# Kernel tuning notes

Hardware: AMD Instinct MI355X
Metric: run time of the kernel (lower is better)

Reference implementation:

```python
import jax, jax.numpy as jnp
import numpy as np

H, W, T = 128, 128, 4
BLOCK_W = 16
N = 1024
CHOL_BOUND = jnp.array([0.5, 0.0, 0.0, 0.5, 0.0, 0.5], dtype=jnp.float32)  # diag lower bound
SCALE = 2.0 * BLOCK_W / W  # gaussian footprint ~ tile-sized in normalized [-1,1] coords


def setup_inputs() -> dict:
    key = jax.random.key(0)
    k1, k2, k3, k4 = jax.random.split(key, 4)
    return {
        "xyz_3D": jax.random.normal(k1, (N, 3), dtype=jnp.float32),
        "cholesky_3D": jax.random.uniform(k2, (N, 6), dtype=jnp.float32),
        "features_dc_3D": jax.random.uniform(k3, (N, 3), dtype=jnp.float32),
        "opacity_3D": jax.random.normal(k4, (N, 1), dtype=jnp.float32),
    }


def _splat(xyz, chol6, feats, opac):
    # activations (match module properties)
    means = jnp.tanh(xyz)                      # [N,3] in [-1,1], (x,y,t)
    c = chol6 + CHOL_BOUND[None, :]            # [N,6]
    alpha_g = jax.nn.sigmoid(opac)             # [N,1]

    # lower-triangular L: rows (x,y,t); layout (0,0)=c0,(1,0)=c1,(2,0)=c2,(1,1)=c3,(2,1)=c4,(2,2)=c5
    zeros = jnp.zeros_like(c[:, 0])
    L = jnp.stack([
        jnp.stack([c[:, 0], zeros,   zeros], -1),
        jnp.stack([c[:, 1], c[:, 3], zeros], -1),
        jnp.stack([c[:, 2], c[:, 4], c[:, 5]], -1),
    ], axis=1) * SCALE                          # [N,3,3]
    Sigma = jnp.einsum('nij,nkj->nik', L, L)    # L L^T, [N,3,3]
    Sinv = jnp.linalg.inv(Sigma)                # [N,3,3]

    # voxel-center grids in normalized [-1,1]
    xs = (jnp.arange(W, dtype=jnp.float32) + 0.5) / W * 2.0 - 1.0
    ys = (jnp.arange(H, dtype=jnp.float32) + 0.5) / H * 2.0 - 1.0
    ts = (jnp.arange(T, dtype=jnp.float32) + 0.5) / T * 2.0 - 1.0

    dx = xs[None, :] - means[:, 0:1]            # [N,W]
    dy = ys[None, :] - means[:, 1:2]            # [N,H]
    dt = ts[None, :] - means[:, 2:3]            # [N,T]

    a  = Sinv[:, 0, 0][:, None, None, None]
    b  = Sinv[:, 1, 1][:, None, None, None]
    cc = Sinv[:, 2, 2][:, None, None, None]
    ab = Sinv[:, 0, 1][:, None, None, None]
    at = Sinv[:, 0, 2][:, None, None, None]
    bt = Sinv[:, 1, 2][:, None, None, None]

    dxw = dx[:, None, None, :]                  # [N,1,1,W]
    dyh = dy[:, None, :, None]                  # [N,1,H,1]
    dtt = dt[:, :, None, None]                  # [N,T,1,1]

    # quadratic form d^T Sigma^{-1} d over the full [N,T,H,W] grid
    q = (a * dxw * dxw + b * dyh * dyh + cc * dtt * dtt
         + 2.0 * ab * dxw * dyh + 2.0 * at * dxw * dtt + 2.0 * bt * dyh * dtt)

    dens = alpha_g[:, :, None, None] * jnp.exp(-0.5 * q)   # [N,T,H,W]
    img = jnp.einsum('nthw,nc->thwc', dens, feats)          # [T,H,W,3]
    return jnp.clip(img, 0.0, 1.0)


def reference(xyz_3D, cholesky_3D, features_dc_3D, opacity_3D):
    return _splat(xyz_3D, cholesky_3D, features_dc_3D, opacity_3D)
```

## Files before the change

### kernel.cpp

```cpp
#include <hip/hip_runtime.h>
#include <hip/hip_fp16.h>


#define GV_H 128
#define GV_W 128
#define GV_T 4
#define GV_NMAX 1024
#define GV_DX 0.015625f
#define K_HALF_LOG2E (-0.72134752044448170f)
#define GV_LOG2E 1.44269504088896340f
#define U_CULL (-20.0f)

typedef float f32x2 __attribute__((ext_vector_type(2)));

__device__ __forceinline__ float fexp2(float x) { return __builtin_amdgcn_exp2f(x); }
__device__ __forceinline__ float frcp(float x)  { return __builtin_amdgcn_rcpf(x); }
__device__ __forceinline__ float flog2(float x) { return __builtin_amdgcn_logf(x); }

__device__ __forceinline__ float fast_tanh(float x) {
    float t = fexp2(2.885390082f * x);
    return fmaf(-2.0f, frcp(t + 1.0f), 1.0f);
}

__global__ __launch_bounds__(1024) void gv_fused_kernel(
    const float* __restrict__ xyz, const float* __restrict__ chol,
    const float* __restrict__ feats, const float* __restrict__ opac,
    float* __restrict__ out, int N)
{
    __shared__ __align__(16) float stab[12800];
    __shared__ int swt[16];

    int b    = blockIdx.x;
    int slab = b & 63;
    int t    = b >> 6;
    int tid  = threadIdx.x;
    int wv   = tid >> 6;
    int lane = tid & 63;

    float y0r = ((float)(slab * 2) + 0.5f) * GV_DX - 1.0f;
    float y1r = y0r + GV_DX;

    float A = 0.f, gy0 = 0.f, gy1 = 0.f, h0 = 0.f, h1 = 0.f, sv = 0.f;
    float rgbits = 0.f, fb = 0.f;
    bool keep = false;

    if (tid < N) {
        int n = tid;
        float mx = fast_tanh(xyz[n * 3 + 0]);
        float my = fast_tanh(xyz[n * 3 + 1]);
        float mt = fast_tanh(xyz[n * 3 + 2]);

        const float sc = 2.0f * 16.0f / (float)GV_W;
        float L00 = sc * (chol[n * 6 + 0] + 0.5f);
        float L10 = sc * (chol[n * 6 + 1]);
        float L20 = sc * (chol[n * 6 + 2]);
        float L11 = sc * (chol[n * 6 + 3] + 0.5f);
        float L21 = sc * (chol[n * 6 + 4]);
        float L22 = sc * (chol[n * 6 + 5] + 0.5f);

        float il0 = frcp(L00), il1 = frcp(L11), il2 = frcp(L22);
        float m10 = -L10 * il0 * il1;
        float m21 = -L21 * il1 * il2;
        float m20 = (L10 * L21 - L11 * L20) * (il0 * il1 * il2);
        float a   = il0 * il0 + m10 * m10 + m20 * m20;
        float sab = m10 * il1 + m20 * m21;
        float sat = m20 * il2;
        float bb  = il1 * il1 + m21 * m21;
        float sbt = m21 * il2;
        float cc  = il2 * il2;
        float ab2 = 2.0f * sab, at2 = 2.0f * sat, bt2 = 2.0f * sbt;

        float o = opac[n];
        float bias = -flog2(1.0f + fexp2(-GV_LOG2E * o));

        float tv = ((float)t + 0.5f) * (2.0f / (float)GV_T) - 1.0f;
        float dt = tv - mt;

        const float k = K_HALF_LOG2E;
        A        = k * a;
        float B  = k * bb;
        float C  = k * ab2;
        float Dx = k * (at2 * dt - 2.0f * a * mx - ab2 * my);
        float Dy = k * (bt2 * dt - 2.0f * bb * my - ab2 * mx);
        float E  = k * (a * mx * mx + bb * my * my + cc * dt * dt
                        + ab2 * mx * my - at2 * mx * dt - bt2 * my * dt) + bias;

        gy0 = fmaf(C, y0r, Dx);
        gy1 = fmaf(C, y1r, Dx);
        h0  = fmaf(fmaf(B, y0r, Dy), y0r, E);
        h1  = fmaf(fmaf(B, y1r, Dy), y1r, E);
        sv  = fexp2(2.0f * A * GV_DX * GV_DX);

        float fr = feats[n * 3 + 0];
        float fg = feats[n * 3 + 1];
        fb       = feats[n * 3 + 2];
        unsigned hr = (unsigned)__half_as_ushort(__float2half_rn(fr))
                    | ((unsigned)__half_as_ushort(__float2half_rn(fg)) << 16);
        rgbits = __uint_as_float(hr);

        float inv2A = 0.5f * frcp(A);
        float xs0 = fminf(fmaxf(-gy0 * inv2A, -1.0f), 1.0f);
        float xs1 = fminf(fmaxf(-gy1 * inv2A, -1.0f), 1.0f);
        float u0  = fmaf(fmaf(A, xs0, gy0), xs0, h0);
        float u1  = fmaf(fmaf(A, xs1, gy1), xs1, h1);
        keep = (fmaxf(u0, u1) > U_CULL);
    }

    unsigned long long bm = __ballot((int)keep);
    int wprefix = __popcll(bm & ((1ull << lane) - 1ull));
    if (lane == 0) swt[wv] = (int)__popcll(bm);
    __syncthreads();

    int base = 0, M = 0;
    #pragma unroll
    for (int k2 = 0; k2 < 16; ++k2) {
        int c = swt[k2];
        if (k2 < wv) base += c;
        M += c;
    }
    if (keep) {
        float4* dst = (float4*)&stab[(base + wprefix) * 8];
        dst[0] = make_float4(gy0, gy1, h0, h1);
        dst[1] = make_float4(A, sv, rgbits, fb);
    }
    int M64 = (M + 63) & ~63;
    if (tid >= M && tid < M64) {
        float4* dst = (float4*)&stab[tid * 8];
        dst[0] = make_float4(0.f, 0.f, -1e30f, -1e30f);
        dst[1] = make_float4(0.f, 0.f, 0.f, 0.f);
    }
    __syncthreads();

    int oct  = lane & 15;
    int slot = lane >> 4;

    float x0  = ((float)(oct * 8) + 0.5f) * GV_DX - 1.0f;
    float caa = 2.0f * x0 + GV_DX;
    f32x2 x02  = { x0, x0 };
    f32x2 caa2 = { caa, caa };
    f32x2 dx2  = { GV_DX, GV_DX };

    int iters = M64 >> 6;
    const float* rp = &stab[(wv * 4 + slot) * 8];

    f32x2 aR2[8], aG2[8], aB2[8];
    #pragma unroll
    for (int j = 0; j < 8; ++j) {
        aR2[j] = (f32x2)(0.f); aG2[j] = (f32x2)(0.f); aB2[j] = (f32x2)(0.f);
    }

    #pragma unroll 1
    for (int it = 0; it < iters; ++it) {
        const float4* q = (const float4*)rp;
        float4 q0 = q[0];
        float4 q1 = q[1];
        rp += 64 * 8;

        f32x2 gy = { q0.x, q0.y };
        f32x2 hh = { q0.z, q0.w };
        f32x2 A2 = { q1.x, q1.x };

        f32x2 u2 = __builtin_elementwise_fma(
                       __builtin_elementwise_fma(A2, x02, gy), x02, hh);
        f32x2 e2 = { fexp2(u2[0]), fexp2(u2[1]) };
        f32x2 ra = __builtin_elementwise_fma(A2, caa2, gy) * dx2;
        f32x2 r2 = { fexp2(ra[0]), fexp2(ra[1]) };
        f32x2 s2 = { q1.y, q1.y };

        unsigned bits = __float_as_uint(q1.z);
        float fr = __half2float(__ushort_as_half((unsigned short)(bits & 0xffffu)));
        float fg = __half2float(__ushort_as_half((unsigned short)(bits >> 16)));
        f32x2 fr2 = { fr, fr };
        f32x2 fg2 = { fg, fg };
        f32x2 fb2 = { q1.w, q1.w };

        #pragma unroll
        for (int j = 0; j < 8; ++j) {
            aR2[j] = __builtin_elementwise_fma(e2, fr2, aR2[j]);
            aG2[j] = __builtin_elementwise_fma(e2, fg2, aG2[j]);
            aB2[j] = __builtin_elementwise_fma(e2, fb2, aB2[j]);
            if (j < 7) { e2 *= r2; r2 *= s2; }
        }
    }

    #pragma unroll
    for (int j = 0; j < 8; ++j) {
        aR2[j][0] += __shfl_xor(aR2[j][0], 16, 64);
        aR2[j][1] += __shfl_xor(aR2[j][1], 16, 64);
        aG2[j][0] += __shfl_xor(aG2[j][0], 16, 64);
        aG2[j][1] += __shfl_xor(aG2[j][1], 16, 64);
        aB2[j][0] += __shfl_xor(aB2[j][0], 16, 64);
        aB2[j][1] += __shfl_xor(aB2[j][1], 16, 64);
        aR2[j][0] += __shfl_xor(aR2[j][0], 32, 64);
        aR2[j][1] += __shfl_xor(aR2[j][1], 32, 64);
        aG2[j][0] += __shfl_xor(aG2[j][0], 32, 64);
        aG2[j][1] += __shfl_xor(aG2[j][1], 32, 64);
        aB2[j][0] += __shfl_xor(aB2[j][0], 32, 64);
        aB2[j][1] += __shfl_xor(aB2[j][1], 32, 64);
    }

    __syncthreads();

    if (slot == 0) {
        f32x2* d2 = (f32x2*)&stab[wv * 800];
        #pragma unroll
        for (int j = 0; j < 8; ++j) {
            d2[oct * 24 + j * 3 + 0] = aR2[j];
            d2[oct * 24 + j * 3 + 1] = aG2[j];
            d2[oct * 24 + j * 3 + 2] = aB2[j];
        }
    }
    __syncthreads();

    if (tid < 2 * GV_W * 3) {
        int o   = tid;
        int c   = o % 3;
        int pxr = o / 3;
        int x   = pxr & 127;
        int row = pxr >> 7;
        int op  = x * 3 + c;
        float sacc = 0.f;
        #pragma unroll
        for (int wvI = 0; wvI < 16; ++wvI)
            sacc += stab[wvI * 800 + op * 2 + row];
        int basew = ((t * GV_H + slab * 2) * GV_W) * 3;
        out[basew + o] = fminf(fmaxf(sacc, 0.0f), 1.0f);
    }
}

extern "C" void kernel_launch(void* const* d_in, const int* in_sizes, int n_in,
                              void* d_out, int out_size, void* d_ws, size_t ws_size,
                              hipStream_t stream) {
    const float* xyz   = (const float*)d_in[0];
    const float* chol  = (const float*)d_in[1];
    const float* feats = (const float*)d_in[2];
    const float* opac  = (const float*)d_in[3];
    float* out = (float*)d_out;
    int N = in_sizes[0] / 3;
    if (N > GV_NMAX) N = GV_NMAX;

    int blocks = GV_T * (GV_H / 2);
    gv_fused_kernel<<<blocks, 1024, 0, stream>>>(xyz, chol, feats, opac, out, N);
}
```

Before: 18.23 us.

## Split each row-pair slab into x-quarters with 512-thread blocks and per-quarter culling

Splits the grid four ways along x, giving 1024 blocks of 512 threads instead of 256 blocks of 1024. Each block culls gaussians against its 32-pixel x range, so fewer survive per block. Threads now handle one row and 8 pixels with two interleaved exp recurrences, which lowers register pressure and lets three blocks share a CU. In exchange, every block recomputes the per-gaussian setup (two gaussians per thread), so total preprocessing work grows fourfold.

```diff
diff --git a/kernel.cpp b/kernel.cpp
--- a/kernel.cpp
+++ b/kernel.cpp
@@ -22,150 +22,177 @@
     return fmaf(-2.0f, frcp(t + 1.0f), 1.0f);
 }
 
-__global__ __launch_bounds__(1024) void gv_fused_kernel(
+__global__ __launch_bounds__(512, 3) void gv_fused_kernel(
     const float* __restrict__ xyz, const float* __restrict__ chol,
     const float* __restrict__ feats, const float* __restrict__ opac,
     float* __restrict__ out, int N)
 {
-    __shared__ __align__(16) float stab[12800];
+    __shared__ __align__(16) float stab[GV_NMAX * 8];
     __shared__ int swt[16];
 
     int b    = blockIdx.x;
-    int slab = b & 63;
-    int t    = b >> 6;
+    int xq   = b & 3;
+    int slab = (b >> 2) & 63;
+    int t    = b >> 8;
     int tid  = threadIdx.x;
     int wv   = tid >> 6;
     int lane = tid & 63;
 
     float y0r = ((float)(slab * 2) + 0.5f) * GV_DX - 1.0f;
     float y1r = y0r + GV_DX;
-
-    float A = 0.f, gy0 = 0.f, gy1 = 0.f, h0 = 0.f, h1 = 0.f, sv = 0.f;
-    float rgbits = 0.f, fb = 0.f;
-    bool keep = false;
-
-    if (tid < N) {
-        int n = tid;
-        float mx = fast_tanh(xyz[n * 3 + 0]);
-        float my = fast_tanh(xyz[n * 3 + 1]);
-        float mt = fast_tanh(xyz[n * 3 + 2]);
-
-        const float sc = 2.0f * 16.0f / (float)GV_W;
-        float L00 = sc * (chol[n * 6 + 0] + 0.5f);
-        float L10 = sc * (chol[n * 6 + 1]);
-        float L20 = sc * (chol[n * 6 + 2]);
-        float L11 = sc * (chol[n * 6 + 3] + 0.5f);
-        float L21 = sc * (chol[n * 6 + 4]);
-        float L22 = sc * (chol[n * 6 + 5] + 0.5f);
-
-        float il0 = frcp(L00), il1 = frcp(L11), il2 = frcp(L22);
-        float m10 = -L10 * il0 * il1;
-        float m21 = -L21 * il1 * il2;
-        float m20 = (L10 * L21 - L11 * L20) * (il0 * il1 * il2);
-        float a   = il0 * il0 + m10 * m10 + m20 * m20;
-        float sab = m10 * il1 + m20 * m21;
-        float sat = m20 * il2;
-        float bb  = il1 * il1 + m21 * m21;
-        float sbt = m21 * il2;
-        float cc  = il2 * il2;
-        float ab2 = 2.0f * sab, at2 = 2.0f * sat, bt2 = 2.0f * sbt;
-
-        float o = opac[n];
-        float bias = -flog2(1.0f + fexp2(-GV_LOG2E * o));
-
-        float tv = ((float)t + 0.5f) * (2.0f / (float)GV_T) - 1.0f;
-        float dt = tv - mt;
-
-        const float k = K_HALF_LOG2E;
-        A        = k * a;
-        float B  = k * bb;
-        float C  = k * ab2;
-        float Dx = k * (at2 * dt - 2.0f * a * mx - ab2 * my);
-        float Dy = k * (bt2 * dt - 2.0f * bb * my - ab2 * mx);
-        float E  = k * (a * mx * mx + bb * my * my + cc * dt * dt
-                        + ab2 * mx * my - at2 * mx * dt - bt2 * my * dt) + bias;
-
-        gy0 = fmaf(C, y0r, Dx);
-        gy1 = fmaf(C, y1r, Dx);
-        h0  = fmaf(fmaf(B, y0r, Dy), y0r, E);
-        h1  = fmaf(fmaf(B, y1r, Dy), y1r, E);
-        sv  = fexp2(2.0f * A * GV_DX * GV_DX);
-
-        float fr = feats[n * 3 + 0];
-        float fg = feats[n * 3 + 1];
-        fb       = feats[n * 3 + 2];
-        unsigned hr = (unsigned)__half_as_ushort(__float2half_rn(fr))
-                    | ((unsigned)__half_as_ushort(__float2half_rn(fg)) << 16);
-        rgbits = __uint_as_float(hr);
-
-        float inv2A = 0.5f * frcp(A);
-        float xs0 = fminf(fmaxf(-gy0 * inv2A, -1.0f), 1.0f);
-        float xs1 = fminf(fmaxf(-gy1 * inv2A, -1.0f), 1.0f);
-        float u0  = fmaf(fmaf(A, xs0, gy0), xs0, h0);
-        float u1  = fmaf(fmaf(A, xs1, gy1), xs1, h1);
-        keep = (fmaxf(u0, u1) > U_CULL);
-    }
-
-    unsigned long long bm = __ballot((int)keep);
-    int wprefix = __popcll(bm & ((1ull << lane) - 1ull));
-    if (lane == 0) swt[wv] = (int)__popcll(bm);
-    __syncthreads();
-
-    int base = 0, M = 0;
+    float xlo = ((float)(xq * 32) + 0.5f) * GV_DX - 1.0f;
+    float xhi = xlo + 31.0f * GV_DX;
+
+    float4 rec0[2], rec1[2];
+    bool keep[2];
+    unsigned long long bm[2];
+
+    #pragma unroll
+    for (int r = 0; r < 2; ++r) {
+        keep[r] = false;
+        rec0[r] = make_float4(0.f, 0.f, -1e30f, -1e30f);
+        rec1[r] = make_float4(0.f, 0.f, 0.f, 0.f);
+        int n = r * 512 + tid;
+        if (n < N) {
+            float mx = fast_tanh(xyz[n * 3 + 0]);
+            float my = fast_tanh(xyz[n * 3 + 1]);
+            float mt = fast_tanh(xyz[n * 3 + 2]);
+
+            const float sc = 2.0f * 16.0f / (float)GV_W;
+            float L00 = sc * (chol[n * 6 + 0] + 0.5f);
+            float L10 = sc * (chol[n * 6 + 1]);
+            float L20 = sc * (chol[n * 6 + 2]);
+            float L11 = sc * (chol[n * 6 + 3] + 0.5f);
+            float L21 = sc * (chol[n * 6 + 4]);
+            float L22 = sc * (chol[n * 6 + 5] + 0.5f);
+
+            float il0 = frcp(L00), il1 = frcp(L11), il2 = frcp(L22);
+            float m10 = -L10 * il0 * il1;
+            float m21 = -L21 * il1 * il2;
+            float m20 = (L10 * L21 - L11 * L20) * (il0 * il1 * il2);
+            float a   = il0 * il0 + m10 * m10 + m20 * m20;
+            float sab = m10 * il1 + m20 * m21;
+            float sat = m20 * il2;
+            float bb  = il1 * il1 + m21 * m21;
+            float sbt = m21 * il2;
+            float cc  = il2 * il2;
+            float ab2 = 2.0f * sab, at2 = 2.0f * sat, bt2 = 2.0f * sbt;
+
+            float o = opac[n];
+            float bias = -flog2(1.0f + fexp2(-GV_LOG2E * o));
+
+            float tv = ((float)t + 0.5f) * (2.0f / (float)GV_T) - 1.0f;
+            float dt = tv - mt;
+
+            const float k = K_HALF_LOG2E;
+            float A  = k * a;
+            float B  = k * bb;
+            float C  = k * ab2;
+            float Dx = k * (at2 * dt - 2.0f * a * mx - ab2 * my);
+            float Dy = k * (bt2 * dt - 2.0f * bb * my - ab2 * mx);
+            float E  = k * (a * mx * mx + bb * my * my + cc * dt * dt
+                            + ab2 * mx * my - at2 * mx * dt - bt2 * my * dt)
+                       + bias;
+
+            float gy0 = fmaf(C, y0r, Dx);
+            float gy1 = fmaf(C, y1r, Dx);
+            float h0  = fmaf(fmaf(B, y0r, Dy), y0r, E);
+            float h1  = fmaf(fmaf(B, y1r, Dy), y1r, E);
+            float ss  = fexp2(A * (8.0f * GV_DX * GV_DX));
+
+            float fr = feats[n * 3 + 0];
+            float fg = feats[n * 3 + 1];
+            float fb = feats[n * 3 + 2];
+            unsigned hr = (unsigned)__half_as_ushort(__float2half_rn(fr))
+                        | ((unsigned)__half_as_ushort(__float2half_rn(fg)) << 16);
+            float rgbits = __uint_as_float(hr);
+
+            float inv2A = 0.5f * frcp(A);
+            float xs0 = fminf(fmaxf(-gy0 * inv2A, xlo), xhi);
+            float xs1 = fminf(fmaxf(-gy1 * inv2A, xlo), xhi);
+            float u0  = fmaf(fmaf(A, xs0, gy0), xs0, h0);
+            float u1  = fmaf(fmaf(A, xs1, gy1), xs1, h1);
+            keep[r] = (fmaxf(u0, u1) > U_CULL);
+
+            rec0[r] = make_float4(gy0, gy1, h0, h1);
+            rec1[r] = make_float4(A, ss, rgbits, fb);
+        }
+        bm[r] = __ballot((int)keep[r]);
+    }
+
+    if (lane == 0) {
+        swt[wv]     = (int)__popcll(bm[0]);
+        swt[8 + wv] = (int)__popcll(bm[1]);
+    }
+    __syncthreads();
+
+    int M = 0, base0 = 0, base1 = 0;
     #pragma unroll
     for (int k2 = 0; k2 < 16; ++k2) {
         int c = swt[k2];
-        if (k2 < wv) base += c;
+        if (k2 < wv)     base0 += c;
+        if (k2 < 8 + wv) base1 += c;
         M += c;
     }
-    if (keep) {
-        float4* dst = (float4*)&stab[(base + wprefix) * 8];
-        dst[0] = make_float4(gy0, gy1, h0, h1);
-        dst[1] = make_float4(A, sv, rgbits, fb);
-    }
-    int M64 = (M + 63) & ~63;
-    if (tid >= M && tid < M64) {
-        float4* dst = (float4*)&stab[tid * 8];
-        dst[0] = make_float4(0.f, 0.f, -1e30f, -1e30f);
-        dst[1] = make_float4(0.f, 0.f, 0.f, 0.f);
-    }
-    __syncthreads();
-
-    int oct  = lane & 15;
-    int slot = lane >> 4;
-
-    float x0  = ((float)(oct * 8) + 0.5f) * GV_DX - 1.0f;
+    unsigned long long lmask = (1ull << lane) - 1ull;
+    if (keep[0]) {
+        float4* dst = (float4*)&stab[(base0 + (int)__popcll(bm[0] & lmask)) * 8];
+        dst[0] = rec0[0]; dst[1] = rec1[0];
+    }
+    if (keep[1]) {
+        float4* dst = (float4*)&stab[(base1 + (int)__popcll(bm[1] & lmask)) * 8];
+        dst[0] = rec0[1]; dst[1] = rec1[1];
+    }
+    int MP = (M + 63) & ~63;
+    #pragma unroll
+    for (int r = 0; r < 2; ++r) {
+        int di = r * 512 + tid;
+        if (di >= M && di < MP) {
+            float4* dst = (float4*)&stab[di * 8];
+            dst[0] = make_float4(0.f, 0.f, -1e30f, -1e30f);
+            dst[1] = make_float4(0.f, 0.f, 0.f, 0.f);
+        }
+    }
+    __syncthreads();
+
+    int slot = lane >> 3;
+    int pg   = lane & 7;
+    int oct  = pg & 3;
+    int row  = pg >> 2;
+
+    float x0  = ((float)(xq * 32 + oct * 8) + 0.5f) * GV_DX - 1.0f;
     float caa = 2.0f * x0 + GV_DX;
-    f32x2 x02  = { x0, x0 };
-    f32x2 caa2 = { caa, caa };
-    f32x2 dx2  = { GV_DX, GV_DX };
-
-    int iters = M64 >> 6;
-    const float* rp = &stab[(wv * 4 + slot) * 8];
-
-    f32x2 aR2[8], aG2[8], aB2[8];
-    #pragma unroll
-    for (int j = 0; j < 8; ++j) {
-        aR2[j] = (f32x2)(0.f); aG2[j] = (f32x2)(0.f); aB2[j] = (f32x2)(0.f);
-    }
+    const float c2d2 = 2.0f * GV_DX * GV_DX;
+    bool r1 = (row == 1);
+
+    f32x2 aR[4], aG[4], aB[4];
+    #pragma unroll
+    for (int j = 0; j < 4; ++j) {
+        aR[j] = (f32x2)(0.f); aG[j] = (f32x2)(0.f); aB[j] = (f32x2)(0.f);
+    }
+
+    int iters = MP >> 6;
+    const float4* rp = (const float4*)&stab[(wv * 8 + slot) * 8];
 
     #pragma unroll 1
     for (int it = 0; it < iters; ++it) {
-        const float4* q = (const float4*)rp;
-        float4 q0 = q[0];
-        float4 q1 = q[1];
-        rp += 64 * 8;
-
-        f32x2 gy = { q0.x, q0.y };
-        f32x2 hh = { q0.z, q0.w };
-        f32x2 A2 = { q1.x, q1.x };
-
-        f32x2 u2 = __builtin_elementwise_fma(
-                       __builtin_elementwise_fma(A2, x02, gy), x02, hh);
-        f32x2 e2 = { fexp2(u2[0]), fexp2(u2[1]) };
-        f32x2 ra = __builtin_elementwise_fma(A2, caa2, gy) * dx2;
-        f32x2 r2 = { fexp2(ra[0]), fexp2(ra[1]) };
-        f32x2 s2 = { q1.y, q1.y };
+        float4 q0 = rp[0];
+        float4 q1 = rp[1];
+        rp += 64 * 2;
+
+        float gy = r1 ? q0.y : q0.x;
+        float h  = r1 ? q0.w : q0.z;
+        float A  = q1.x;
+
+        float u0 = fmaf(fmaf(A, x0, gy), x0, h);
+        float d0 = GV_DX * fmaf(A, caa, gy);
+        float t1 = A * c2d2;
+        float p0 = fmaf(2.0f, d0, t1);
+        float p1 = fmaf(2.0f, t1, p0);
+
+        f32x2 e2  = { fexp2(u0), fexp2(u0 + d0) };
+        f32x2 rr2 = { fexp2(p0), fexp2(p1) };
+        f32x2 ss2 = { q1.y, q1.y };
 
         unsigned bits = __float_as_uint(q1.z);
         float fr = __half2float(__ushort_as_half((unsigned short)(bits & 0xffffu)));
@@ -175,56 +202,58 @@
         f32x2 fb2 = { q1.w, q1.w };
 
         #pragma unroll
-        for (int j = 0; j < 8; ++j) {
-            aR2[j] = __builtin_elementwise_fma(e2, fr2, aR2[j]);
-            aG2[j] = __builtin_elementwise_fma(e2, fg2, aG2[j]);
-            aB2[j] = __builtin_elementwise_fma(e2, fb2, aB2[j]);
-            if (j < 7) { e2 *= r2; r2 *= s2; }
-        }
-    }
-
-    #pragma unroll
-    for (int j = 0; j < 8; ++j) {
-        aR2[j][0] += __shfl_xor(aR2[j][0], 16, 64);
-        aR2[j][1] += __shfl_xor(aR2[j][1], 16, 64);
-        aG2[j][0] += __shfl_xor(aG2[j][0], 16, 64);
-        aG2[j][1] += __shfl_xor(aG2[j][1], 16, 64);
-        aB2[j][0] += __shfl_xor(aB2[j][0], 16, 64);
-        aB2[j][1] += __shfl_xor(aB2[j][1], 16, 64);
-        aR2[j][0] += __shfl_xor(aR2[j][0], 32, 64);
-        aR2[j][1] += __shfl_xor(aR2[j][1], 32, 64);
-        aG2[j][0] += __shfl_xor(aG2[j][0], 32, 64);
-        aG2[j][1] += __shfl_xor(aG2[j][1], 32, 64);
-        aB2[j][0] += __shfl_xor(aB2[j][0], 32, 64);
-        aB2[j][1] += __shfl_xor(aB2[j][1], 32, 64);
+        for (int j = 0; j < 4; ++j) {
+            aR[j] = __builtin_elementwise_fma(e2, fr2, aR[j]);
+            aG[j] = __builtin_elementwise_fma(e2, fg2, aG[j]);
+            aB[j] = __builtin_elementwise_fma(e2, fb2, aB[j]);
+            if (j < 3) { e2 *= rr2; rr2 *= ss2; }
+        }
+    }
+
+    #pragma unroll
+    for (int j = 0; j < 4; ++j) {
+        #pragma unroll
+        for (int m = 8; m <= 32; m <<= 1) {
+            aR[j][0] += __shfl_xor(aR[j][0], m, 64);
+            aR[j][1] += __shfl_xor(aR[j][1], m, 64);
+            aG[j][0] += __shfl_xor(aG[j][0], m, 64);
+            aG[j][1] += __shfl_xor(aG[j][1], m, 64);
+            aB[j][0] += __shfl_xor(aB[j][0], m, 64);
+            aB[j][1] += __shfl_xor(aB[j][1], m, 64);
+        }
     }
 
     __syncthreads();
 
     if (slot == 0) {
-        f32x2* d2 = (f32x2*)&stab[wv * 800];
-        #pragma unroll
-        for (int j = 0; j < 8; ++j) {
-            d2[oct * 24 + j * 3 + 0] = aR2[j];
-            d2[oct * 24 + j * 3 + 1] = aG2[j];
-            d2[oct * 24 + j * 3 + 2] = aB2[j];
-        }
-    }
-    __syncthreads();
-
-    if (tid < 2 * GV_W * 3) {
-        int o   = tid;
-        int c   = o % 3;
-        int pxr = o / 3;
-        int x   = pxr & 127;
-        int row = pxr >> 7;
-        int op  = x * 3 + c;
-        float sacc = 0.f;
-        #pragma unroll
-        for (int wvI = 0; wvI < 16; ++wvI)
-            sacc += stab[wvI * 800 + op * 2 + row];
-        int basew = ((t * GV_H + slab * 2) * GV_W) * 3;
-        out[basew + o] = fminf(fmaxf(sacc, 0.0f), 1.0f);
+        float* dst = &stab[wv * 208 + pg * 26];
+        #pragma unroll
+        for (int j = 0; j < 4; ++j) {
+            dst[j * 6 + 0] = aR[j][0];
+            dst[j * 6 + 1] = aR[j][1];
+            dst[j * 6 + 2] = aG[j][0];
+            dst[j * 6 + 3] = aG[j][1];
+            dst[j * 6 + 4] = aB[j][0];
+            dst[j * 6 + 5] = aB[j][1];
+        }
+    }
+    __syncthreads();
+
+    if (tid < 192) {
+        int c   = tid % 3;
+        int px  = tid / 3;
+        int x   = px & 31;
+        int rw  = px >> 5;
+        int oc  = x >> 3;
+        int p8  = x & 7;
+        int j   = p8 >> 1;
+        int cmp = p8 & 1;
+        int ofs = (rw * 4 + oc) * 26 + j * 6 + c * 2 + cmp;
+        float sum = 0.f;
+        #pragma unroll
+        for (int w = 0; w < 8; ++w) sum += stab[w * 208 + ofs];
+        int idx = ((t * GV_H + slab * 2 + rw) * GV_W + xq * 32 + x) * 3 + c;
+        out[idx] = fminf(fmaxf(sum, 0.0f), 1.0f);
     }
 }
 
@@ -239,6 +268,6 @@
     int N = in_sizes[0] / 3;
     if (N > GV_NMAX) N = GV_NMAX;
 
-    int blocks = GV_T * (GV_H / 2);
-    gv_fused_kernel<<<blocks, 1024, 0, stream>>>(xyz, chol, feats, opac, out, N);
+    int blocks = GV_T * 64 * 4;
+    gv_fused_kernel<<<blocks, 512, 0, stream>>>(xyz, chol, feats, opac, out, N);
 }
```

Measured after the change: 21.15 us. 1.16x slower.
